# Kernel optimization log

Measured on AMD Instinct MI355X. Metric: run time of the kernel, lower is better.

## Reference

```python
import jax, jax.numpy as jnp
import numpy as np

NUM_HEADS = 16
HEAD_DIM = 64  # dim_qkv // num_heads


def setup_inputs() -> dict:
    key = jax.random.key(0)
    ks = jax.random.split(key, 6)
    B, N, D = 2, 2048, 1024
    s = 1.0 / np.sqrt(D)
    x = jax.random.normal(ks[0], (B, N, D), dtype=jnp.float32)
    Wq = jax.random.normal(ks[1], (D, D), dtype=jnp.float32) * s
    Wk = jax.random.normal(ks[2], (D, D), dtype=jnp.float32) * s
    Wv = jax.random.normal(ks[3], (D, D), dtype=jnp.float32) * s
    Wo = jax.random.normal(ks[4], (D, D), dtype=jnp.float32) * s
    z = jnp.zeros((D,), dtype=jnp.float32)
    return {"x": x, "Wq": Wq, "bq": z, "Wk": Wk, "bk": z,
            "Wv": Wv, "bv": z, "Wo": Wo, "bo": z}


def _split_heads(t):
    # [B, N, H*dh] -> [B, H, N, dh]
    B, N, _ = t.shape
    return t.reshape(B, N, NUM_HEADS, HEAD_DIM).transpose(0, 2, 1, 3)


def reference(x, Wq, bq, Wk, bk, Wv, bv, Wo, bo):
    q = _split_heads(x @ Wq + bq)
    k = _split_heads(x @ Wk + bk)
    v = _split_heads(x @ Wv + bv)
    scores = jnp.einsum('bhnd,bhmd->bhnm', q, k) / jnp.sqrt(
        jnp.asarray(HEAD_DIM, dtype=x.dtype))
    attn = jax.nn.softmax(scores, axis=-1)
    heads = jnp.einsum('bhnm,bhmd->bhnd', attn, v)  # [B, H, N, dh]
    B, H, N, dh = heads.shape
    merged = heads.transpose(0, 2, 1, 3).reshape(B, N, H * dh)
    # dropout is identity in deterministic/eval mode
    return merged @ Wo + bo
```

## Files before the change

kernel.cpp:

```cpp
#include <hip/hip_runtime.h>
#include <hip/hip_bf16.h>

typedef __bf16 bf16;
typedef __attribute__((ext_vector_type(8))) __bf16 bf16x8;
typedef __attribute__((ext_vector_type(4))) __bf16 bf16x4;
typedef __attribute__((ext_vector_type(4))) float f32x4;
typedef __attribute__((ext_vector_type(16))) float f32x16;
typedef unsigned int uint;

#define MFMA16(a, b, c) __builtin_amdgcn_mfma_f32_16x16x32_bf16(a, b, c, 0, 0, 0)
#define MFMA32(a, b, c) __builtin_amdgcn_mfma_f32_32x32x16_bf16(a, b, c, 0, 0, 0)

#define GLOAD_LDS(gp, lp) \
  __builtin_amdgcn_global_load_lds( \
      (const __attribute__((address_space(1))) void*)(gp), \
      (__attribute__((address_space(3))) void*)(lp), 16, 0, 0)

#define QSCALE 0.18033688011112042f

__device__ __forceinline__ uint pack2(float a, float b) {
  unsigned short x = __builtin_bit_cast(unsigned short, (bf16)a);
  unsigned short y = __builtin_bit_cast(unsigned short, (bf16)b);
  return (uint)x | ((uint)y << 16);
}

__global__ __launch_bounds__(256) void prep_kernel(
    const float* __restrict__ x, bf16* __restrict__ y,
    const float* __restrict__ W0, const float* __restrict__ W1,
    const float* __restrict__ W2, const float* __restrict__ W3,
    bf16* __restrict__ T0, bf16* __restrict__ T1,
    bf16* __restrict__ T2, bf16* __restrict__ T3) {
  const int bid = blockIdx.x;
  if (bid < 2048) {
    int i = (bid * 256 + threadIdx.x) * 8;
    float4 a = *(const float4*)(x + i);
    float4 b = *(const float4*)(x + i + 4);
    bf16x8 v;
    v[0] = (bf16)a.x; v[1] = (bf16)a.y; v[2] = (bf16)a.z; v[3] = (bf16)a.w;
    v[4] = (bf16)b.x; v[5] = (bf16)b.y; v[6] = (bf16)b.z; v[7] = (bf16)b.w;
    *(bf16x8*)(y + i) = v;
    return;
  }
  const int wq = bid - 2048;
  const int z = wq >> 10, rem = wq & 1023;
  const float* W; bf16* T;
  switch (z) {
    case 0: W = W0; T = T0; break;
    case 1: W = W1; T = T1; break;
    case 2: W = W2; T = T2; break;
    default: W = W3; T = T3; break;
  }
  const float scl = (z == 0) ? QSCALE : 1.0f;
  __shared__ float tile[32][33];
  int tx = threadIdx.x & 31;
  int ty = threadIdx.x >> 5;
  int bx = (rem & 31) * 32, by = (rem >> 5) * 32;
#pragma unroll
  for (int i = 0; i < 32; i += 8)
    tile[ty + i][tx] = W[(size_t)(by + ty + i) * 1024 + bx + tx];
  __syncthreads();
#pragma unroll
  for (int i = 0; i < 32; i += 8)
    T[(size_t)(bx + ty + i) * 1024 + by + tx] = (bf16)(tile[tx][ty + i] * scl);
}

__global__ __launch_bounds__(256, 2) void gemm_qkv_kernel(
    const bf16* __restrict__ A, const bf16* __restrict__ Bt,
    const float* __restrict__ b0, const float* __restrict__ b1,
    const float* __restrict__ b2, bf16* __restrict__ o0,
    bf16* __restrict__ o1, bf16* __restrict__ o2) {
  __shared__ bf16 As[128 * 64];
  __shared__ bf16 Bs[128 * 64];
  const int f = blockIdx.y * 24 + blockIdx.x;
  const int wg = (f % 8) * 96 + f / 8;
  const int bn = wg % 24, bm = wg / 24;
  const int t = threadIdx.x;
  const int lane = t & 63, wid = t >> 6;
  const int wy = wid >> 1, wx = wid & 1;
  const int lr = lane & 15, lg = lane >> 4;
  const bf16* Arow = A + (size_t)bm * 128 * 1024;
  const bf16* Brow = Bt + (size_t)bn * 128 * 1024;
  f32x4 acc[4][4] = {};

  for (int k0 = 0; k0 < 1024; k0 += 64) {
    __syncthreads();
#pragma unroll
    for (int i = 0; i < 4; i++) {
      int off = i * 256 + t;
      int row = off >> 3, ch = off & 7;
      int gch = ch ^ (row & 7);
      GLOAD_LDS(Arow + (size_t)row * 1024 + k0 + gch * 8, As + off * 8);
    }
#pragma unroll
    for (int i = 0; i < 4; i++) {
      int off = i * 256 + t;
      int row = off >> 3, ch = off & 7;
      int gch = ch ^ (row & 7);
      GLOAD_LDS(Brow + (size_t)row * 1024 + k0 + gch * 8, Bs + off * 8);
    }
    __syncthreads();
#pragma unroll
    for (int kh = 0; kh < 2; kh++) {
      bf16x8 af[4], bfr[4];
#pragma unroll
      for (int i = 0; i < 4; i++) {
        int row = wy * 64 + i * 16 + lr;
        int c = kh * 4 + lg;
        af[i] = *(const bf16x8*)(As + row * 64 + ((c ^ (row & 7)) << 3));
      }
#pragma unroll
      for (int j = 0; j < 4; j++) {
        int row = wx * 64 + j * 16 + lr;
        int c = kh * 4 + lg;
        bfr[j] = *(const bf16x8*)(Bs + row * 64 + ((c ^ (row & 7)) << 3));
      }
#pragma unroll
      for (int i = 0; i < 4; i++)
#pragma unroll
        for (int j = 0; j < 4; j++)
          acc[i][j] = MFMA16(af[i], bfr[j], acc[i][j]);
    }
  }

  const int seg = bn >> 3;
  const float* bias = (seg == 0) ? b0 : (seg == 1 ? b1 : b2);
  const float bscale = (seg == 0) ? QSCALE : 1.0f;

#pragma unroll
  for (int i = 0; i < 4; i++) {
    const int rowb = bm * 128 + wy * 64 + i * 16 + lg * 4;
#pragma unroll
    for (int j = 0; j < 4; j++) {
      const int np = bn * 128 + wx * 64 + j * 16 + lr;
      const int col = np & 1023;
      const float bv = bias[col] * bscale;
      const int h = col >> 6, d = col & 63;
      const int bb = rowb >> 11, nn = rowb & 2047;
      if (seg == 2) {
        bf16x4 pk;
#pragma unroll
        for (int r = 0; r < 4; r++) pk[r] = (bf16)(acc[i][j][r] + bv);
        *(bf16x4*)(o2 + (((size_t)bb * 16 + h) * 64 + d) * 2048 + nn) = pk;
      } else {
        bf16* dst = (seg == 0) ? o0 : o1;
#pragma unroll
        for (int r = 0; r < 4; r++)
          dst[(((size_t)bb * 16 + h) * 2048 + nn + r) * 64 + d] =
              (bf16)(acc[i][j][r] + bv);
      }
    }
  }
}

__global__ __launch_bounds__(256, 2) void gemmo_kernel(
    const bf16* __restrict__ A, const bf16* __restrict__ Bt,
    const float* __restrict__ bias, float* __restrict__ out) {
  __shared__ bf16 As[128 * 64];
  __shared__ bf16 Bs[64 * 64];
  const int f = blockIdx.y * 16 + blockIdx.x;
  const int wg = (f & 7) * 64 + (f >> 3);
  const int bn = wg & 15, bm = wg >> 4;
  const int t = threadIdx.x;
  const int lane = t & 63, wid = t >> 6;
  const int wy = wid >> 1, wx = wid & 1;
  const int lr = lane & 15, lg = lane >> 4;
  const bf16* Arow = A + (size_t)bm * 128 * 1024;
  const bf16* Brow = Bt + (size_t)bn * 64 * 1024;
  f32x4 acc[4][2] = {};

  for (int k0 = 0; k0 < 1024; k0 += 64) {
    __syncthreads();
#pragma unroll
    for (int i = 0; i < 4; i++) {
      int off = i * 256 + t;
      int row = off >> 3, ch = off & 7;
      int gch = ch ^ (row & 7);
      GLOAD_LDS(Arow + (size_t)row * 1024 + k0 + gch * 8, As + off * 8);
    }
#pragma unroll
    for (int i = 0; i < 2; i++) {
      int off = i * 256 + t;
      int row = off >> 3, ch = off & 7;
      int gch = ch ^ (row & 7);
      GLOAD_LDS(Brow + (size_t)row * 1024 + k0 + gch * 8, Bs + off * 8);
    }
    __syncthreads();
#pragma unroll
    for (int kh = 0; kh < 2; kh++) {
      bf16x8 af[4], bfr[2];
#pragma unroll
      for (int i = 0; i < 4; i++) {
        int row = wy * 64 + i * 16 + lr;
        int c = kh * 4 + lg;
        af[i] = *(const bf16x8*)(As + row * 64 + ((c ^ (row & 7)) << 3));
      }
#pragma unroll
      for (int j = 0; j < 2; j++) {
        int row = wx * 32 + j * 16 + lr;
        int c = kh * 4 + lg;
        bfr[j] = *(const bf16x8*)(Bs + row * 64 + ((c ^ (row & 7)) << 3));
      }
#pragma unroll
      for (int i = 0; i < 4; i++)
#pragma unroll
        for (int j = 0; j < 2; j++)
          acc[i][j] = MFMA16(af[i], bfr[j], acc[i][j]);
    }
  }

#pragma unroll
  for (int i = 0; i < 4; i++) {
    const int rowb = bm * 128 + wy * 64 + i * 16 + lg * 4;
#pragma unroll
    for (int j = 0; j < 2; j++) {
      const int col = bn * 64 + wx * 32 + j * 16 + lr;
      const float bv = bias[col];
#pragma unroll
      for (int r = 0; r < 4; r++)
        out[(size_t)(rowb + r) * 1024 + col] = acc[i][j][r] + bv;
    }
  }
}

__global__ __launch_bounds__(256, 2) void attn_kernel(
    const bf16* __restrict__ Q, const bf16* __restrict__ K,
    const bf16* __restrict__ Vt, bf16* __restrict__ Mg) {
  __shared__ bf16 Kl[2][8192];
  __shared__ bf16 Vl[2][8192];
  const int t = threadIdx.x;
  const int lane = t & 63, w = t >> 6;
  const int l31 = lane & 31, hi = lane >> 5;
  const int f = blockIdx.y * 16 + blockIdx.x;
  const int xcd = f & 7, slot = f >> 3;
  const int bh = xcd * 4 + (slot >> 4);
  const int bx = slot & 15;
  const int b = bh >> 4, h = bh & 15;
  const bf16* Qh = Q + (size_t)bh * 2048 * 64;
  const bf16* Kh = K + (size_t)bh * 2048 * 64;
  const bf16* Vh = Vt + (size_t)bh * 64 * 2048;
  const int q_row = bx * 128 + w * 32 + l31;

  bf16x8 qf[4];
#pragma unroll
  for (int dblk = 0; dblk < 4; dblk++)
    qf[dblk] = *(const bf16x8*)(Qh + (size_t)q_row * 64 + dblk * 16 + hi * 8);

  f32x16 o0 = {}, o1 = {};
  float lrun = 0.f;

#define STAGE(kt_, buf_)                                                      \
  {                                                                           \
    _Pragma("unroll") for (int i = 0; i < 4; i++) {                           \
      int off = i * 256 + t;                                                  \
      int row = off >> 3, ch = off & 7;                                       \
      int gch = ch ^ (row & 7);                                               \
      GLOAD_LDS(Kh + (size_t)(kt_) * 8192 + row * 64 + gch * 8,               \
                &Kl[buf_][off * 8]);                                          \
    }                                                                         \
    _Pragma("unroll") for (int i = 0; i < 4; i++) {                           \
      int off = i * 256 + t;                                                  \
      int row = off >> 4, ch = off & 15;                                      \
      int gch = ch ^ (row & 15);                                              \
      GLOAD_LDS(Vh + (size_t)row * 2048 + (kt_) * 128 + gch * 8,              \
                &Vl[buf_][off * 8]);                                          \
    }                                                                         \
  }

  STAGE(0, 0);
  __syncthreads();

  for (int kt = 0; kt < 16; kt++) {
    const int cur = kt & 1;
    if (kt < 15) STAGE(kt + 1, cur ^ 1);

    f32x16 s[4] = {{0}, {0}, {0}, {0}};
#pragma unroll
    for (int dblk = 0; dblk < 4; dblk++) {
      const int c = dblk * 2 + hi;
#pragma unroll
      for (int rg = 0; rg < 4; rg++) {
        const int row = rg * 32 + l31;
        bf16x8 kf = *(const bf16x8*)&Kl[cur][row * 64 + ((c ^ (row & 7)) << 3)];
        s[rg] = MFMA32(kf, qf[dblk], s[rg]);
      }
    }

    float rs = 0.f;
#pragma unroll
    for (int rg = 0; rg < 4; rg++)
#pragma unroll
      for (int r = 0; r < 16; r++) {
        s[rg][r] = __builtin_amdgcn_exp2f(s[rg][r]);
        rs += s[rg][r];
      }
    rs += __shfl_xor(rs, 32);
    lrun += rs;

    uint prc[16], prd[16];
#pragma unroll
    for (int g = 0; g < 4; g++)
#pragma unroll
      for (int si = 0; si < 4; si++) {
        prc[g * 4 + si] = pack2(s[g][4 * si + 0], s[g][4 * si + 1]);
        prd[g * 4 + si] = pack2(s[g][4 * si + 2], s[g][4 * si + 3]);
      }

#pragma unroll
    for (int kb = 0; kb < 8; kb++) {
      const int sb = (kb >> 1) * 4 + (kb & 1) * 2;
      uint sendc = hi ? prc[sb] : prc[sb + 1];
      uint sendd = hi ? prd[sb] : prd[sb + 1];
      uint recvc = __shfl_xor(sendc, 32);
      uint recvd = __shfl_xor(sendd, 32);
      union { uint u[4]; bf16x8 v; } pf;
      pf.u[0] = hi ? recvc : prc[sb];
      pf.u[1] = hi ? recvd : prd[sb];
      pf.u[2] = hi ? prc[sb + 1] : recvc;
      pf.u[3] = hi ? prd[sb + 1] : recvd;

      const int c = kb * 2 + hi;
      bf16x8 vt0 = *(const bf16x8*)&Vl[cur][l31 * 128 + ((c ^ (l31 & 15)) << 3)];
      bf16x8 vt1 =
          *(const bf16x8*)&Vl[cur][(32 + l31) * 128 + ((c ^ ((32 + l31) & 15)) << 3)];
      o0 = MFMA32(vt0, pf.v, o0);
      o1 = MFMA32(vt1, pf.v, o1);
    }

    __syncthreads();
  }

  const float inv = 1.f / lrun;
  bf16* orow = Mg + ((size_t)b * 2048 + q_row) * 1024 + h * 64;
#pragma unroll
  for (int si = 0; si < 4; si++) {
    bf16x4 p0, p1;
#pragma unroll
    for (int r = 0; r < 4; r++) {
      p0[r] = (bf16)(o0[4 * si + r] * inv);
      p1[r] = (bf16)(o1[4 * si + r] * inv);
    }
    *(bf16x4*)(orow + si * 8 + hi * 4) = p0;
    *(bf16x4*)(orow + 32 + si * 8 + hi * 4) = p1;
  }
}

extern "C" void kernel_launch(void* const* d_in, const int* in_sizes, int n_in,
                              void* d_out, int out_size, void* d_ws, size_t ws_size,
                              hipStream_t stream) {
  const float* x  = (const float*)d_in[0];
  const float* Wq = (const float*)d_in[1];
  const float* bq = (const float*)d_in[2];
  const float* Wk = (const float*)d_in[3];
  const float* bk = (const float*)d_in[4];
  const float* Wv = (const float*)d_in[5];
  const float* bv = (const float*)d_in[6];
  const float* Wo = (const float*)d_in[7];
  const float* bo = (const float*)d_in[8];
  float* out = (float*)d_out;
  char* ws = (char*)d_ws;
  const size_t MiB = 1u << 20;

  bf16* Xb   = (bf16*)(ws);
  bf16* Mg   = Xb;
  bf16* Wqkv = (bf16*)(ws + 8 * MiB);
  bf16* WoT  = (bf16*)(ws + 14 * MiB);
  bf16* Qb   = (bf16*)(ws + 16 * MiB);
  bf16* Kb   = (bf16*)(ws + 24 * MiB);
  bf16* Vtb  = (bf16*)(ws + 32 * MiB);

  prep_kernel<<<6144, 256, 0, stream>>>(
      x, Xb, Wq, Wk, Wv, Wo, Wqkv, Wqkv + (1u << 20), Wqkv + (2u << 20), WoT);
  gemm_qkv_kernel<<<dim3(24, 32), 256, 0, stream>>>(
      Xb, Wqkv, bq, bk, bv, Qb, Kb, Vtb);
  attn_kernel<<<dim3(16, 32), 256, 0, stream>>>(Qb, Kb, Vtb, Mg);
  gemmo_kernel<<<dim3(16, 32), 256, 0, stream>>>(Mg, WoT, bo, out);
  (void)in_sizes; (void)n_in; (void)out_size; (void)ws_size;
}
```

Baseline: 113.3 us.

## Split attention tile into halves, use permlane32 swap and MFMA row-sum

Processes each 128-key tile in two 64-key halves to lower live score registers. Replaces the shfl_xor exchange with permlane32_swap and computes the softmax denominator with an extra MFMA against a ones vector instead of scalar adds. Also raises wave priority around the MFMA blocks with s_setprio. This adds one MFMA per PV step and relies on the bf16-rounded P values for the row sum, which slightly changes numerics.

```diff
diff --git a/kernel.cpp b/kernel.cpp
--- a/kernel.cpp
+++ b/kernel.cpp
@@ -245,8 +245,14 @@
   for (int dblk = 0; dblk < 4; dblk++)
     qf[dblk] = *(const bf16x8*)(Qh + (size_t)q_row * 64 + dblk * 16 + hi * 8);
 
-  f32x16 o0 = {}, o1 = {};
-  float lrun = 0.f;
+  bf16x8 onesA;
+  {
+    bf16 ov = (l31 == 0) ? (bf16)1.0f : (bf16)0.0f;
+#pragma unroll
+    for (int e = 0; e < 8; e++) onesA[e] = ov;
+  }
+
+  f32x16 o0 = {}, o1 = {}, osum = {};
 
 #define STAGE(kt_, buf_)                                                      \
   {                                                                           \
@@ -273,63 +279,66 @@
     const int cur = kt & 1;
     if (kt < 15) STAGE(kt + 1, cur ^ 1);
 
-    f32x16 s[4] = {{0}, {0}, {0}, {0}};
-#pragma unroll
-    for (int dblk = 0; dblk < 4; dblk++) {
-      const int c = dblk * 2 + hi;
-#pragma unroll
-      for (int rg = 0; rg < 4; rg++) {
-        const int row = rg * 32 + l31;
-        bf16x8 kf = *(const bf16x8*)&Kl[cur][row * 64 + ((c ^ (row & 7)) << 3)];
-        s[rg] = MFMA32(kf, qf[dblk], s[rg]);
-      }
-    }
-
-    float rs = 0.f;
-#pragma unroll
-    for (int rg = 0; rg < 4; rg++)
+#pragma unroll
+    for (int hf = 0; hf < 2; hf++) {
+      f32x16 s0 = {}, s1 = {};
+      __builtin_amdgcn_s_setprio(1);
+#pragma unroll
+      for (int dblk = 0; dblk < 4; dblk++) {
+        const int c = dblk * 2 + hi;
+        const int r0 = hf * 64 + l31, r1 = hf * 64 + 32 + l31;
+        bf16x8 kf0 = *(const bf16x8*)&Kl[cur][r0 * 64 + ((c ^ (r0 & 7)) << 3)];
+        bf16x8 kf1 = *(const bf16x8*)&Kl[cur][r1 * 64 + ((c ^ (r1 & 7)) << 3)];
+        s0 = MFMA32(kf0, qf[dblk], s0);
+        s1 = MFMA32(kf1, qf[dblk], s1);
+      }
+      __builtin_amdgcn_s_setprio(0);
+
 #pragma unroll
       for (int r = 0; r < 16; r++) {
-        s[rg][r] = __builtin_amdgcn_exp2f(s[rg][r]);
-        rs += s[rg][r];
-      }
-    rs += __shfl_xor(rs, 32);
-    lrun += rs;
-
-    uint prc[16], prd[16];
-#pragma unroll
-    for (int g = 0; g < 4; g++)
+        s0[r] = __builtin_amdgcn_exp2f(s0[r]);
+        s1[r] = __builtin_amdgcn_exp2f(s1[r]);
+      }
+
+      uint prc[8], prd[8];
 #pragma unroll
       for (int si = 0; si < 4; si++) {
-        prc[g * 4 + si] = pack2(s[g][4 * si + 0], s[g][4 * si + 1]);
-        prd[g * 4 + si] = pack2(s[g][4 * si + 2], s[g][4 * si + 3]);
-      }
-
-#pragma unroll
-    for (int kb = 0; kb < 8; kb++) {
-      const int sb = (kb >> 1) * 4 + (kb & 1) * 2;
-      uint sendc = hi ? prc[sb] : prc[sb + 1];
-      uint sendd = hi ? prd[sb] : prd[sb + 1];
-      uint recvc = __shfl_xor(sendc, 32);
-      uint recvd = __shfl_xor(sendd, 32);
-      union { uint u[4]; bf16x8 v; } pf;
-      pf.u[0] = hi ? recvc : prc[sb];
-      pf.u[1] = hi ? recvd : prd[sb];
-      pf.u[2] = hi ? prc[sb + 1] : recvc;
-      pf.u[3] = hi ? prd[sb + 1] : recvd;
-
-      const int c = kb * 2 + hi;
-      bf16x8 vt0 = *(const bf16x8*)&Vl[cur][l31 * 128 + ((c ^ (l31 & 15)) << 3)];
-      bf16x8 vt1 =
-          *(const bf16x8*)&Vl[cur][(32 + l31) * 128 + ((c ^ ((32 + l31) & 15)) << 3)];
-      o0 = MFMA32(vt0, pf.v, o0);
-      o1 = MFMA32(vt1, pf.v, o1);
-    }
-
-    __syncthreads();
-  }
-
-  const float inv = 1.f / lrun;
+        prc[si] = pack2(s0[4 * si + 0], s0[4 * si + 1]);
+        prd[si] = pack2(s0[4 * si + 2], s0[4 * si + 3]);
+        prc[4 + si] = pack2(s1[4 * si + 0], s1[4 * si + 1]);
+        prd[4 + si] = pack2(s1[4 * si + 2], s1[4 * si + 3]);
+      }
+
+      __builtin_amdgcn_s_setprio(1);
+#pragma unroll
+      for (int kbl = 0; kbl < 4; kbl++) {
+        const int sb = (kbl >> 1) * 4 + (kbl & 1) * 2;
+        auto rc = __builtin_amdgcn_permlane32_swap(prc[sb], prc[sb + 1], false, false);
+        auto rd = __builtin_amdgcn_permlane32_swap(prd[sb], prd[sb + 1], false, false);
+        union { uint u[4]; bf16x8 v; } pf;
+        pf.u[0] = rc[0];
+        pf.u[1] = rd[0];
+        pf.u[2] = rc[1];
+        pf.u[3] = rd[1];
+
+        const int c = (hf * 4 + kbl) * 2 + hi;
+        bf16x8 vt0 = *(const bf16x8*)&Vl[cur][l31 * 128 + ((c ^ (l31 & 15)) << 3)];
+        bf16x8 vt1 =
+            *(const bf16x8*)&Vl[cur][(32 + l31) * 128 + ((c ^ ((32 + l31) & 15)) << 3)];
+        o0 = MFMA32(vt0, pf.v, o0);
+        o1 = MFMA32(vt1, pf.v, o1);
+        osum = MFMA32(onesA, pf.v, osum);
+      }
+      __builtin_amdgcn_s_setprio(0);
+    }
+
+    __syncthreads();
+  }
+
+  uint lu = __builtin_bit_cast(uint, osum[0]);
+  auto lb = __builtin_amdgcn_permlane32_swap(lu, lu, false, false);
+  const float inv = 1.f / __builtin_bit_cast(float, (uint)lb[0]);
+
   bf16* orow = Mg + ((size_t)b * 2048 + q_row) * 1024 + h * 64;
 #pragma unroll
   for (int si = 0; si < 4; si++) {
```

Result: no change. 111.6 us (-1.5%).
